# Kernel tuning notes

Hardware: AMD Instinct MI355X
Metric: run time of the kernel (lower is better)

## Reference

```python
import jax, jax.numpy as jnp
import numpy as np

NEG_SLOPE = 0.2


def gat_conv(x, edge_index, W, a_src, a_dst, b, heads, ch, concat):
    # PyG GATConv (eval mode, add_self_loops=True).
    # x: [N, Fin]; W: [Fin, heads*ch]; a_src/a_dst: [heads, ch]; b: [heads*ch] or [ch]
    N = x.shape[0]
    loop = jnp.arange(N, dtype=edge_index.dtype)
    src = jnp.concatenate([edge_index[0], loop])
    dst = jnp.concatenate([edge_index[1], loop])
    h = (x @ W).reshape(N, heads, ch)                     # [N,H,C]
    s_src = jnp.sum(h * a_src, axis=-1)                   # [N,H]
    s_dst = jnp.sum(h * a_dst, axis=-1)                   # [N,H]
    e = jax.nn.leaky_relu(s_src[src] + s_dst[dst], NEG_SLOPE)  # [E,H]
    # numerically stable softmax over incoming edges of each dst node
    emax = jax.lax.stop_gradient(jax.ops.segment_max(e, dst, num_segments=N))
    ex = jnp.exp(e - emax[dst])
    denom = jax.ops.segment_sum(ex, dst, num_segments=N) + 1e-16
    alpha = ex / denom[dst]                                # [E,H]
    out = jax.ops.segment_sum(alpha[:, :, None] * h[src], dst, num_segments=N)  # [N,H,C]
    out = out.reshape(N, heads * ch) if concat else out.mean(axis=1)
    return out + b


def setup_inputs() -> dict:
    key = jax.random.key(0)
    N, E, Fin, H, C = 50000, 800000, 64, 8, 16
    D1 = H * C            # 128
    D2 = 3 * D1           # 384
    ks = jax.random.split(key, 40)
    d = {}
    d["X"] = jax.random.normal(ks[0], (N, Fin), dtype=jnp.float32)
    d["A1"] = jax.random.randint(ks[1], (2, E), 0, N, dtype=jnp.int32)
    d["A2"] = jax.random.randint(ks[2], (2, E), 0, N, dtype=jnp.int32)
    d["A3"] = jax.random.randint(ks[3], (2, E), 0, N, dtype=jnp.int32)
    d["edge_feature"] = jax.random.normal(ks[4], (E, 2), dtype=jnp.float32)
    i = 5
    for branch in (1, 2, 3):
        d[f"W{branch}1"] = jax.random.normal(ks[i], (Fin, D1), dtype=jnp.float32) * 0.1; i += 1
        d[f"a_src{branch}1"] = jax.random.normal(ks[i], (H, C), dtype=jnp.float32) * 0.1; i += 1
        d[f"a_dst{branch}1"] = jax.random.normal(ks[i], (H, C), dtype=jnp.float32) * 0.1; i += 1
        d[f"b{branch}1"] = jnp.zeros((D1,), dtype=jnp.float32)
        d[f"W{branch}2"] = jax.random.normal(ks[i], (D2, 1), dtype=jnp.float32) * 0.1; i += 1
        d[f"a_src{branch}2"] = jax.random.normal(ks[i], (1, 1), dtype=jnp.float32) * 0.1; i += 1
        d[f"a_dst{branch}2"] = jax.random.normal(ks[i], (1, 1), dtype=jnp.float32) * 0.1; i += 1
        d[f"b{branch}2"] = jnp.zeros((1,), dtype=jnp.float32)
    d["ln_w"] = jax.random.normal(ks[i], (3, 1), dtype=jnp.float32) * 0.1
    d["ln_b"] = jnp.zeros((1,), dtype=jnp.float32)
    return d


def reference(X, A1, A2, A3, edge_feature,
              W11, a_src11, a_dst11, b11, W12, a_src12, a_dst12, b12,
              W21, a_src21, a_dst21, b21, W22, a_src22, a_dst22, b22,
              W31, a_src31, a_dst31, b31, W32, a_src32, a_dst32, b32,
              ln_w, ln_b):
    H, C = 8, 16
    X1 = jax.nn.relu(gat_conv(X, A1, W11, a_src11, a_dst11, b11, H, C, True))
    X2 = jax.nn.relu(gat_conv(X, A2, W21, a_src21, a_dst21, b21, H, C, True))
    X3 = jax.nn.relu(gat_conv(X, A3, W31, a_src31, a_dst31, b31, H, C, True))
    Xc = jnp.concatenate([X1, X2, X3], axis=1)            # [N, 384]
    Y1 = gat_conv(Xc, A1, W12, a_src12, a_dst12, b12, 1, 1, False)
    Y2 = gat_conv(Xc, A2, W22, a_src22, a_dst22, b22, 1, 1, False)
    Y3 = gat_conv(Xc, A3, W32, a_src32, a_dst32, b32, 1, 1, False)
    Y = jnp.concatenate([Y1, Y2, Y3], axis=1)             # [N, 3]
    return Y @ ln_w + ln_b                                # [N, 1]
```

## Files before the change

kernel.cpp:

```cpp
#include <hip/hip_runtime.h>
#include <cstdint>
#include <cstddef>

#define NEG_SLOPE 0.2f
#define L1_NODES 64
#define EPT 32
#define EPB (384 * EPT)

__device__ __forceinline__ float lrelu(float v) { return v >= 0.f ? v : NEG_SLOPE * v; }

__device__ __forceinline__ unsigned short f2bf(float x) {
    union { float f; uint32_t u; } v; v.f = x;
    uint32_t r = v.u + 0x7FFFu + ((v.u >> 16) & 1u);
    return (unsigned short)(r >> 16);
}
__device__ __forceinline__ float bf2f_lo(uint32_t u) {
    union { uint32_t u; float f; } v; v.u = u << 16;
    return v.f;
}
__device__ __forceinline__ float bf2f_hi(uint32_t u) {
    union { uint32_t u; float f; } v; v.u = u & 0xFFFF0000u;
    return v.f;
}

__global__ __launch_bounds__(384) void k_p1(
        const int* __restrict__ A1, const int* __restrict__ A2,
        const int* __restrict__ A3,
        int* __restrict__ bofs, float* __restrict__ h2,
        int nbP, int NB, int E, int N) {
    __shared__ int hist[512];
    int t = threadIdx.x, blk = blockIdx.x, r = blockIdx.y;
    for (int i = t; i < NB; i += 384) hist[i] = 0;
    {
        int id = (r * nbP + blk) * 384 + t;
        int stride = 3 * nbP * 384;
        for (int i = id; i < 3 * N; i += stride) h2[i] = 0.f;
    }
    __syncthreads();
    const int* A = (r == 0) ? A1 : (r == 1) ? A2 : A3;
    int base = blk * EPB;
    #pragma unroll
    for (int it = 0; it < EPT; ++it) {
        int e = base + it * 384 + t;
        if (e < E) atomicAdd(&hist[A[E + e] >> 7], 1);
    }
    __syncthreads();
    for (int i = t; i < NB; i += 384)
        bofs[(size_t)(r * nbP + blk) * NB + i] = hist[i];
}

__global__ __launch_bounds__(512) void k_p2a(
        int* __restrict__ bofs, int* __restrict__ gbkt, int nbP, int NB) {
    __shared__ int arr[512];
    int t = threadIdx.x, b = blockIdx.x, r = blockIdx.y;
    int v = (t < nbP) ? bofs[(size_t)(r * nbP + t) * NB + b] : 0;
    arr[t] = v; __syncthreads();
    for (int off = 1; off < 512; off <<= 1) {
        int x = (t >= off) ? arr[t - off] : 0; __syncthreads();
        arr[t] += x; __syncthreads();
    }
    if (t < nbP) bofs[(size_t)(r * nbP + t) * NB + b] = arr[t] - v;
    if (t == 0) gbkt[r * NB + b] = arr[511];
}

__global__ __launch_bounds__(512) void k_p2b(
        const int* __restrict__ gbkt, int* __restrict__ gstart, int NB) {
    __shared__ int arr[512];
    int t = threadIdx.x;
    for (int r = 0; r < 3; ++r) {
        int v = (t < NB) ? gbkt[r * NB + t] : 0;
        arr[t] = v; __syncthreads();
        for (int off = 1; off < 512; off <<= 1) {
            int x = (t >= off) ? arr[t - off] : 0; __syncthreads();
            arr[t] += x; __syncthreads();
        }
        if (t < NB) gstart[r * NB + t] = arr[t] - v;
        __syncthreads();
    }
}

__global__ __launch_bounds__(384) void k_p3_lin1(
        const float* __restrict__ X,
        const float* __restrict__ W1, const float* __restrict__ W2,
        const float* __restrict__ W3,
        const float* __restrict__ as1, const float* __restrict__ ad1,
        const float* __restrict__ as2, const float* __restrict__ ad2,
        const float* __restrict__ as3, const float* __restrict__ ad3,
        unsigned short* __restrict__ h_bf,
        float* __restrict__ s_src, float* __restrict__ s_dst,
        const int* __restrict__ A1, const int* __restrict__ A2,
        const int* __restrict__ A3,
        const int* __restrict__ bofs, const int* __restrict__ gstart,
        uint32_t* __restrict__ ebuf,
        int nL1, int nbP, int NB, int E, int N) {
    int t = threadIdx.x;
    if (blockIdx.x >= (unsigned)nL1) {
        __shared__ int cur[512];
        int b2 = blockIdx.x - nL1;
        int r = b2 / nbP, blk = b2 - r * nbP;
        for (int i = t; i < NB; i += 384) cur[i] = 0;
        __syncthreads();
        const int* A = (r == 0) ? A1 : (r == 1) ? A2 : A3;
        int base = blk * EPB;
        const int* bo = bofs + (size_t)(r * nbP + blk) * NB;
        const int* gs = gstart + r * NB;
        uint32_t* eb = ebuf + (size_t)r * E;
        #pragma unroll 4
        for (int it = 0; it < EPT; ++it) {
            int e = base + it * 384 + t;
            if (e < E) {
                int dst = A[E + e], src = A[e];
                int b = dst >> 7;
                int rank = atomicAdd(&cur[b], 1);
                int pos = gs[b] + bo[b] + rank;
                eb[pos] = ((uint32_t)src << 7) | (uint32_t)(dst & 127);
            }
        }
        return;
    }
    __shared__ float Xs[L1_NODES][64];
    int n0 = blockIdx.x * L1_NODES;
    {
        const float4* X4 = reinterpret_cast<const float4*>(X);
        float4* Xs4 = reinterpret_cast<float4*>(&Xs[0][0]);
        for (int i = t; i < L1_NODES * 16; i += 384) {
            int nl = i >> 4;
            float4 xv = make_float4(0.f, 0.f, 0.f, 0.f);
            if (n0 + nl < N) xv = X4[(size_t)(n0 + nl) * 16 + (i & 15)];
            Xs4[i] = xv;
        }
    }
    int r = t >> 7, col = t & 127, head = (t >> 4) & 7, c = t & 15;
    const float* Wp = ((r == 0) ? W1 : (r == 1) ? W2 : W3) + col;
    float Wc[64];
    #pragma unroll
    for (int k = 0; k < 64; ++k) Wc[k] = Wp[(size_t)k * 128];
    float as_v = ((r == 0) ? as1 : (r == 1) ? as2 : as3)[head * 16 + c];
    float ad_v = ((r == 0) ? ad1 : (r == 1) ? ad2 : ad3)[head * 16 + c];
    __syncthreads();
    int nmax = min(L1_NODES, N - n0);
    int rh = (r << 3) + head;
    for (int n = 0; n < nmax; ++n) {
        const float4* xr = reinterpret_cast<const float4*>(&Xs[n][0]);
        float a0 = 0.f, a1 = 0.f, a2 = 0.f, a3 = 0.f;
        #pragma unroll
        for (int k4 = 0; k4 < 16; ++k4) {
            float4 xv = xr[k4];
            a0 = fmaf(xv.x, Wc[k4 * 4 + 0], a0);
            a1 = fmaf(xv.y, Wc[k4 * 4 + 1], a1);
            a2 = fmaf(xv.z, Wc[k4 * 4 + 2], a2);
            a3 = fmaf(xv.w, Wc[k4 * 4 + 3], a3);
        }
        float acc = (a0 + a1) + (a2 + a3);
        h_bf[(size_t)(n0 + n) * 384 + t] = f2bf(acc);
        float ss = acc * as_v, sd = acc * ad_v;
        ss += __shfl_xor(ss, 1); ss += __shfl_xor(ss, 2);
        ss += __shfl_xor(ss, 4); ss += __shfl_xor(ss, 8);
        sd += __shfl_xor(sd, 1); sd += __shfl_xor(sd, 2);
        sd += __shfl_xor(sd, 4); sd += __shfl_xor(sd, 8);
        if (c == 0) {
            s_src[(size_t)(n0 + n) * 24 + rh] = ss;
            s_dst[(size_t)(n0 + n) * 24 + rh] = sd;
        }
    }
}

__global__ __launch_bounds__(512) void k_p4(
        const uint32_t* __restrict__ ebuf,
        const int* __restrict__ gstart, const int* __restrict__ gbkt,
        unsigned short* __restrict__ csr,
        int* __restrict__ deg, int* __restrict__ start,
        int NB, int E, int N) {
    __shared__ int dcnt[128], dst_[128], dcur[128], tmp[128];
    int t = threadIdx.x, b = blockIdx.x, r = blockIdx.y;
    if (t < 128) { dcnt[t] = 0; dcur[t] = 0; }
    __syncthreads();
    int base = gstart[r * NB + b];
    int m    = gbkt[r * NB + b];
    const uint32_t* eb = ebuf + (size_t)r * E + base;
    for (int i = t; i < m; i += 512) atomicAdd(&dcnt[eb[i] & 127], 1);
    __syncthreads();
    if (t < 128) tmp[t] = dcnt[t];
    __syncthreads();
    #pragma unroll
    for (int off = 1; off < 128; off <<= 1) {
        int x = (t < 128 && t >= off) ? tmp[t - off] : 0; __syncthreads();
        if (t < 128) tmp[t] += x; __syncthreads();
    }
    if (t < 128) {
        dst_[t] = tmp[t] - dcnt[t];
        int node = b * 128 + t;
        if (node < N) {
            deg[(size_t)r * N + node]   = dcnt[t];
            start[(size_t)r * N + node] = base + dst_[t];
        }
    }
    __syncthreads();
    unsigned short* cs = csr + (size_t)r * E + base;
    for (int i = t; i < m; i += 512) {
        uint32_t u = eb[i];
        int dl = u & 127;
        int rank = atomicAdd(&dcur[dl], 1);
        cs[dst_[dl] + rank] = (unsigned short)(u >> 7);
    }
}

__global__ __launch_bounds__(64) void k_agg1(
        const unsigned short* __restrict__ h_bf,
        const float* __restrict__ s_src, const float* __restrict__ s_dst,
        const int* __restrict__ deg, const int* __restrict__ start,
        const unsigned short* __restrict__ csr,
        const float* __restrict__ b1, const float* __restrict__ b2,
        const float* __restrict__ b3,
        const float* __restrict__ W12, const float* __restrict__ W22,
        const float* __restrict__ W32,
        float* __restrict__ h2, int E, int N) {
    __shared__ int sidx[64];
    __shared__ float sex[64 * 8];
    int n = blockIdx.x;
    int r = blockIdx.y;
    int j = threadIdx.x;
    int h = j >> 3;
    int rh = r * 8 + h;
    int s0 = start[(size_t)r * N + n];
    int d  = deg[(size_t)r * N + n];
    const uint32_t* hb = reinterpret_cast<const uint32_t*>(h_bf);
    int off = r * 64 + j;
    float sd = s_dst[(size_t)n * 24 + rh];
    float ex0 = __expf(lrelu(s_src[(size_t)n * 24 + rh] + sd));
    float denom = ex0;
    uint32_t hv0 = hb[(size_t)n * 192 + off];
    float accx = ex0 * bf2f_lo(hv0);
    float accy = ex0 * bf2f_hi(hv0);
    int hA = j & 7;
    float sdA = s_dst[(size_t)n * 24 + r * 8 + hA];
    const unsigned short* cs = csr + (size_t)r * E + s0;
    for (int c0 = 0; c0 < d; c0 += 64) {
        int dc = min(64, d - c0);
        if (j < dc) sidx[j] = cs[c0 + j];
        __syncthreads();
        for (int p = j; p < dc * 8; p += 64) {
            int i = p >> 3;
            float ssv = s_src[(size_t)sidx[i] * 24 + r * 8 + hA];
            sex[p] = __expf(lrelu(ssv + sdA));
        }
        __syncthreads();
        for (int i = 0; i < dc; ++i) {
            float ex = sex[i * 8 + h];
            uint32_t hv = hb[(size_t)sidx[i] * 192 + off];
            denom += ex;
            accx = fmaf(ex, bf2f_lo(hv), accx);
            accy = fmaf(ex, bf2f_hi(hv), accy);
        }
        __syncthreads();
    }
    const float* b = (r == 0) ? b1 : (r == 1) ? b2 : b3;
    float inv = 1.0f / (denom + 1e-16f);
    float ox = accx * inv + b[2 * j];
    float oy = accy * inv + b[2 * j + 1];
    ox = (ox > 0.f) ? ox : 0.f;
    oy = (oy > 0.f) ? oy : 0.f;
    int cbase = r * 128 + 2 * j;
    float p0 = ox * W12[cbase] + oy * W12[cbase + 1];
    float p1 = ox * W22[cbase] + oy * W22[cbase + 1];
    float p2 = ox * W32[cbase] + oy * W32[cbase + 1];
    #pragma unroll
    for (int o = 32; o > 0; o >>= 1) {
        p0 += __shfl_xor(p0, o);
        p1 += __shfl_xor(p1, o);
        p2 += __shfl_xor(p2, o);
    }
    if (j == 0) {
        atomicAdd(&h2[(size_t)n * 3 + 0], p0);
        atomicAdd(&h2[(size_t)n * 3 + 1], p1);
        atomicAdd(&h2[(size_t)n * 3 + 2], p2);
    }
}

__global__ __launch_bounds__(384) void k_agg2f(
        const float* __restrict__ h2,
        const int* __restrict__ deg, const int* __restrict__ start,
        const unsigned short* __restrict__ csr,
        const float* __restrict__ as1, const float* __restrict__ ad1,
        const float* __restrict__ as2, const float* __restrict__ ad2,
        const float* __restrict__ as3, const float* __restrict__ ad3,
        const float* __restrict__ b1, const float* __restrict__ b2,
        const float* __restrict__ b3,
        const float* __restrict__ ln_w, const float* __restrict__ ln_b,
        float* __restrict__ out, int E, int N) {
    __shared__ float ys[48];
    int tl = threadIdx.x;
    int pl = tl >> 3;
    int q  = tl & 7;
    int id = blockIdx.x * 48 + pl;
    bool valid = id < 3 * N;
    int n = id / 3;
    int r = id - 3 * n;
    float denom = 0.f, acc = 0.f;
    if (valid) {
        float a_s = ((r == 0) ? as1 : (r == 1) ? as2 : as3)[0];
        float a_d = ((r == 0) ? ad1 : (r == 1) ? ad2 : ad3)[0];
        int s0 = start[(size_t)r * N + n];
        int d  = deg[(size_t)r * N + n];
        float hd = h2[id];
        float sd = a_d * hd;
        const unsigned short* cs = csr + (size_t)r * E + s0;
        for (int i = q; i < d; i += 8) {
            float hs = h2[(size_t)cs[i] * 3 + r];
            float e2 = __expf(lrelu(fmaf(a_s, hs, sd)));
            denom += e2;
            acc = fmaf(e2, hs, acc);
        }
        if (q == 0) {
            float ev = __expf(lrelu(fmaf(a_s, hd, sd)));
            denom += ev;
            acc = fmaf(ev, hd, acc);
        }
    }
    denom += __shfl_xor(denom, 1); denom += __shfl_xor(denom, 2); denom += __shfl_xor(denom, 4);
    acc   += __shfl_xor(acc, 1);   acc   += __shfl_xor(acc, 2);   acc   += __shfl_xor(acc, 4);
    if (valid && q == 0) {
        float b = ((r == 0) ? b1 : (r == 1) ? b2 : b3)[0];
        ys[pl] = (acc / (denom + 1e-16f) + b) * ln_w[r];
    }
    __syncthreads();
    if (valid && q == 0 && r == 0)
        out[n] = ys[pl] + ys[pl + 1] + ys[pl + 2] + ln_b[0];
}

extern "C" void kernel_launch(void* const* d_in, const int* in_sizes, int n_in,
                              void* d_out, int out_size, void* d_ws, size_t ws_size,
                              hipStream_t stream) {
    const float* X  = (const float*)d_in[0];
    const int*   A1 = (const int*)d_in[1];
    const int*   A2 = (const int*)d_in[2];
    const int*   A3 = (const int*)d_in[3];
    const float* W11 = (const float*)d_in[5];
    const float* as11 = (const float*)d_in[6];
    const float* ad11 = (const float*)d_in[7];
    const float* b11 = (const float*)d_in[8];
    const float* W12 = (const float*)d_in[9];
    const float* as12 = (const float*)d_in[10];
    const float* ad12 = (const float*)d_in[11];
    const float* b12 = (const float*)d_in[12];
    const float* W21 = (const float*)d_in[13];
    const float* as21 = (const float*)d_in[14];
    const float* ad21 = (const float*)d_in[15];
    const float* b21 = (const float*)d_in[16];
    const float* W22 = (const float*)d_in[17];
    const float* as22 = (const float*)d_in[18];
    const float* ad22 = (const float*)d_in[19];
    const float* b22 = (const float*)d_in[20];
    const float* W31 = (const float*)d_in[21];
    const float* as31 = (const float*)d_in[22];
    const float* ad31 = (const float*)d_in[23];
    const float* b31 = (const float*)d_in[24];
    const float* W32 = (const float*)d_in[25];
    const float* as32 = (const float*)d_in[26];
    const float* ad32 = (const float*)d_in[27];
    const float* b32 = (const float*)d_in[28];
    const float* ln_w = (const float*)d_in[29];
    const float* ln_b = (const float*)d_in[30];

    const int N = in_sizes[0] / 64;
    const int E = in_sizes[1] / 2;
    const int NB  = (N + 127) >> 7;
    const int nbP = (E + EPB - 1) / EPB;
    const int nL1 = (N + L1_NODES - 1) / L1_NODES;

    float* w = (float*)d_ws;
    float* s_src1 = w; w += (size_t)N * 24;
    float* s_dst1 = w; w += (size_t)N * 24;
    float* h2     = w; w += (size_t)N * 3;
    unsigned short* h_bf = (unsigned short*)w; w += (size_t)N * 192;
    int* iw     = (int*)w;
    int* deg    = iw; iw += (size_t)3 * N;
    int* start  = iw; iw += (size_t)3 * N;
    int* gbkt   = iw; iw += (size_t)3 * NB;
    int* gstart = iw; iw += (size_t)3 * NB;
    int* bofs   = iw; iw += (size_t)3 * nbP * NB;
    uint32_t* ebuf = (uint32_t*)iw; iw += (size_t)3 * E;
    unsigned short* csr = (unsigned short*)iw;

    k_p1<<<dim3(nbP, 3), 384, 0, stream>>>(A1, A2, A3, bofs, h2, nbP, NB, E, N);
    k_p2a<<<dim3(NB, 3), 512, 0, stream>>>(bofs, gbkt, nbP, NB);
    k_p2b<<<1, 512, 0, stream>>>(gbkt, gstart, NB);
    k_p3_lin1<<<nL1 + 3 * nbP, 384, 0, stream>>>(
        X, W11, W21, W31, as11, ad11, as21, ad21, as31, ad31,
        h_bf, s_src1, s_dst1,
        A1, A2, A3, bofs, gstart, ebuf, nL1, nbP, NB, E, N);
    k_p4<<<dim3(NB, 3), 512, 0, stream>>>(ebuf, gstart, gbkt, csr, deg, start, NB, E, N);

    {
        dim3 grid(N, 3);
        k_agg1<<<grid, 64, 0, stream>>>(h_bf, s_src1, s_dst1, deg, start, csr,
                                        b11, b21, b31, W12, W22, W32, h2, E, N);
    }

    {
        int nb = (3 * N + 47) / 48;
        k_agg2f<<<nb, 384, 0, stream>>>(
            h2, deg, start, csr,
            as12, ad12, as22, ad22, as32, ad32,
            b12, b22, b32, ln_w, ln_b, (float*)d_out, E, N);
    }
}
```

Before: 322.6 us.

## Replace multi-pass bucket scan with fixed-capacity atomic bucket scatter

Drops the separate histogram kernel and two prefix-scan kernels. Each scatter block now builds its own local bucket histogram and reserves space in fixed-capacity per-bucket slots (CAP entries) through global atomics. A single small scan then gives CSR starts, and the bucket sort reads from the fixed-stride buffer. This cuts kernel launches and an extra pass over the edge lists, but it assumes no bucket holds more than CAP edges and makes the edge order inside a bucket nondeterministic.

Result: no change. 316.6 us, median of 2 (-1.9%).

```diff
diff --git a/kernel.cpp b/kernel.cpp
--- a/kernel.cpp
+++ b/kernel.cpp
@@ -6,6 +6,7 @@
 #define L1_NODES 64
 #define EPT 32
 #define EPB (384 * EPT)
+#define CAP 6144
 
 __device__ __forceinline__ float lrelu(float v) { return v >= 0.f ? v : NEG_SLOPE * v; }
 
@@ -23,63 +24,7 @@
     return v.f;
 }
 
-__global__ __launch_bounds__(384) void k_p1(
-        const int* __restrict__ A1, const int* __restrict__ A2,
-        const int* __restrict__ A3,
-        int* __restrict__ bofs, float* __restrict__ h2,
-        int nbP, int NB, int E, int N) {
-    __shared__ int hist[512];
-    int t = threadIdx.x, blk = blockIdx.x, r = blockIdx.y;
-    for (int i = t; i < NB; i += 384) hist[i] = 0;
-    {
-        int id = (r * nbP + blk) * 384 + t;
-        int stride = 3 * nbP * 384;
-        for (int i = id; i < 3 * N; i += stride) h2[i] = 0.f;
-    }
-    __syncthreads();
-    const int* A = (r == 0) ? A1 : (r == 1) ? A2 : A3;
-    int base = blk * EPB;
-    #pragma unroll
-    for (int it = 0; it < EPT; ++it) {
-        int e = base + it * 384 + t;
-        if (e < E) atomicAdd(&hist[A[E + e] >> 7], 1);
-    }
-    __syncthreads();
-    for (int i = t; i < NB; i += 384)
-        bofs[(size_t)(r * nbP + blk) * NB + i] = hist[i];
-}
-
-__global__ __launch_bounds__(512) void k_p2a(
-        int* __restrict__ bofs, int* __restrict__ gbkt, int nbP, int NB) {
-    __shared__ int arr[512];
-    int t = threadIdx.x, b = blockIdx.x, r = blockIdx.y;
-    int v = (t < nbP) ? bofs[(size_t)(r * nbP + t) * NB + b] : 0;
-    arr[t] = v; __syncthreads();
-    for (int off = 1; off < 512; off <<= 1) {
-        int x = (t >= off) ? arr[t - off] : 0; __syncthreads();
-        arr[t] += x; __syncthreads();
-    }
-    if (t < nbP) bofs[(size_t)(r * nbP + t) * NB + b] = arr[t] - v;
-    if (t == 0) gbkt[r * NB + b] = arr[511];
-}
-
-__global__ __launch_bounds__(512) void k_p2b(
-        const int* __restrict__ gbkt, int* __restrict__ gstart, int NB) {
-    __shared__ int arr[512];
-    int t = threadIdx.x;
-    for (int r = 0; r < 3; ++r) {
-        int v = (t < NB) ? gbkt[r * NB + t] : 0;
-        arr[t] = v; __syncthreads();
-        for (int off = 1; off < 512; off <<= 1) {
-            int x = (t >= off) ? arr[t - off] : 0; __syncthreads();
-            arr[t] += x; __syncthreads();
-        }
-        if (t < NB) gstart[r * NB + t] = arr[t] - v;
-        __syncthreads();
-    }
-}
-
-__global__ __launch_bounds__(384) void k_p3_lin1(
+__global__ __launch_bounds__(384) void k_sc_lin1(
         const float* __restrict__ X,
         const float* __restrict__ W1, const float* __restrict__ W2,
         const float* __restrict__ W3,
@@ -90,35 +35,49 @@
         float* __restrict__ s_src, float* __restrict__ s_dst,
         const int* __restrict__ A1, const int* __restrict__ A2,
         const int* __restrict__ A3,
-        const int* __restrict__ bofs, const int* __restrict__ gstart,
-        uint32_t* __restrict__ ebuf,
+        int* __restrict__ bktcnt, uint32_t* __restrict__ ebuf,
+        float* __restrict__ h2,
         int nL1, int nbP, int NB, int E, int N) {
+    __shared__ char smem[16384];
     int t = threadIdx.x;
     if (blockIdx.x >= (unsigned)nL1) {
-        __shared__ int cur[512];
+        int* hist = reinterpret_cast<int*>(smem);
+        int* cur  = hist + 512;
         int b2 = blockIdx.x - nL1;
         int r = b2 / nbP, blk = b2 - r * nbP;
-        for (int i = t; i < NB; i += 384) cur[i] = 0;
+        {
+            int gid = b2 * 384 + t, gstride = 3 * nbP * 384;
+            for (int i = gid; i < 3 * N; i += gstride) h2[i] = 0.f;
+        }
+        for (int i = t; i < NB; i += 384) hist[i] = 0;
         __syncthreads();
         const int* A = (r == 0) ? A1 : (r == 1) ? A2 : A3;
         int base = blk * EPB;
-        const int* bo = bofs + (size_t)(r * nbP + blk) * NB;
-        const int* gs = gstart + r * NB;
-        uint32_t* eb = ebuf + (size_t)r * E;
+        #pragma unroll 4
+        for (int it = 0; it < EPT; ++it) {
+            int e = base + it * 384 + t;
+            if (e < E) atomicAdd(&hist[A[E + e] >> 7], 1);
+        }
+        __syncthreads();
+        for (int i = t; i < NB; i += 384) {
+            int c = hist[i];
+            cur[i] = c ? atomicAdd(&bktcnt[r * NB + i], c) : 0;
+        }
+        __syncthreads();
         #pragma unroll 4
         for (int it = 0; it < EPT; ++it) {
             int e = base + it * 384 + t;
             if (e < E) {
                 int dst = A[E + e], src = A[e];
                 int b = dst >> 7;
-                int rank = atomicAdd(&cur[b], 1);
-                int pos = gs[b] + bo[b] + rank;
-                eb[pos] = ((uint32_t)src << 7) | (uint32_t)(dst & 127);
+                int pos = atomicAdd(&cur[b], 1);
+                ebuf[(size_t)(r * NB + b) * CAP + pos] =
+                    ((uint32_t)src << 7) | (uint32_t)(dst & 127);
             }
         }
         return;
     }
-    __shared__ float Xs[L1_NODES][64];
+    float (*Xs)[64] = reinterpret_cast<float(*)[64]>(smem);
     int n0 = blockIdx.x * L1_NODES;
     {
         const float4* X4 = reinterpret_cast<const float4*>(X);
@@ -165,9 +124,25 @@
     }
 }
 
+__global__ __launch_bounds__(512) void k_scan(
+        const int* __restrict__ bktcnt, int* __restrict__ gstart, int NB) {
+    __shared__ int arr[512];
+    int t = threadIdx.x;
+    for (int r = 0; r < 3; ++r) {
+        int v = (t < NB) ? bktcnt[r * NB + t] : 0;
+        arr[t] = v; __syncthreads();
+        for (int off = 1; off < 512; off <<= 1) {
+            int x = (t >= off) ? arr[t - off] : 0; __syncthreads();
+            arr[t] += x; __syncthreads();
+        }
+        if (t < NB) gstart[r * NB + t] = arr[t] - v;
+        __syncthreads();
+    }
+}
+
 __global__ __launch_bounds__(512) void k_p4(
         const uint32_t* __restrict__ ebuf,
-        const int* __restrict__ gstart, const int* __restrict__ gbkt,
+        const int* __restrict__ gstart, const int* __restrict__ bktcnt,
         unsigned short* __restrict__ csr,
         int* __restrict__ deg, int* __restrict__ start,
         int NB, int E, int N) {
@@ -176,8 +151,8 @@
     if (t < 128) { dcnt[t] = 0; dcur[t] = 0; }
     __syncthreads();
     int base = gstart[r * NB + b];
-    int m    = gbkt[r * NB + b];
-    const uint32_t* eb = ebuf + (size_t)r * E + base;
+    int m    = bktcnt[r * NB + b];
+    const uint32_t* eb = ebuf + (size_t)(r * NB + b) * CAP;
     for (int i = t; i < m; i += 512) atomicAdd(&dcnt[eb[i] & 127], 1);
     __syncthreads();
     if (t < 128) tmp[t] = dcnt[t];
@@ -376,20 +351,20 @@
     int* iw     = (int*)w;
     int* deg    = iw; iw += (size_t)3 * N;
     int* start  = iw; iw += (size_t)3 * N;
-    int* gbkt   = iw; iw += (size_t)3 * NB;
+    int* bktcnt = iw; iw += (size_t)3 * NB;
     int* gstart = iw; iw += (size_t)3 * NB;
-    int* bofs   = iw; iw += (size_t)3 * nbP * NB;
-    uint32_t* ebuf = (uint32_t*)iw; iw += (size_t)3 * E;
+    uint32_t* ebuf = (uint32_t*)iw; iw += (size_t)3 * NB * CAP;
     unsigned short* csr = (unsigned short*)iw;
 
-    k_p1<<<dim3(nbP, 3), 384, 0, stream>>>(A1, A2, A3, bofs, h2, nbP, NB, E, N);
-    k_p2a<<<dim3(NB, 3), 512, 0, stream>>>(bofs, gbkt, nbP, NB);
-    k_p2b<<<1, 512, 0, stream>>>(gbkt, gstart, NB);
-    k_p3_lin1<<<nL1 + 3 * nbP, 384, 0, stream>>>(
+    hipMemsetAsync(bktcnt, 0, (size_t)3 * NB * sizeof(int), stream);
+
+    k_sc_lin1<<<nL1 + 3 * nbP, 384, 0, stream>>>(
         X, W11, W21, W31, as11, ad11, as21, ad21, as31, ad31,
         h_bf, s_src1, s_dst1,
-        A1, A2, A3, bofs, gstart, ebuf, nL1, nbP, NB, E, N);
-    k_p4<<<dim3(NB, 3), 512, 0, stream>>>(ebuf, gstart, gbkt, csr, deg, start, NB, E, N);
+        A1, A2, A3, bktcnt, ebuf, h2, nL1, nbP, NB, E, N);
+
+    k_scan<<<1, 512, 0, stream>>>(bktcnt, gstart, NB);
+    k_p4<<<dim3(NB, 3), 512, 0, stream>>>(ebuf, gstart, bktcnt, csr, deg, start, NB, E, N);
 
     {
         dim3 grid(N, 3);
```
